# Performance work log

Measured on AMD Instinct MI355X. Metric: run time of the kernel, lower is better.

## Reference

```python
import jax, jax.numpy as jnp
import numpy as np

EPS = 1e-5


def layer_norm(x, g, b):
    mu = jnp.mean(x, axis=-1, keepdims=True)
    var = jnp.mean((x - mu) ** 2, axis=-1, keepdims=True)
    return (x - mu) * jax.lax.rsqrt(var + EPS) * g + b


def rel_enc_shift(arr):
    # Transformer-XL shift trick: [b,n,l,m] -> shifted [b,n,l,m]
    b, n, l, m = arr.shape
    arr = jnp.concatenate([arr, jnp.zeros((b, n, l, 1), arr.dtype)], axis=-1)
    arr = arr.reshape(b, n, -1)
    arr = arr[:, :, l - 1:-1].reshape(b, n, l, m)
    return arr


def setup_inputs() -> dict:
    key = jax.random.key(0)
    B, S, M, D, H = 2, 1024, 1024, 1024, 16
    F = S + M
    ks = jax.random.split(key, 16)
    sc = 0.02
    inp = {
        "inputs": jax.random.normal(ks[0], (B, S, D), jnp.float32),
        "mem": jax.random.normal(ks[1], (B, M, D), jnp.float32),
        "rel_enc": jax.random.normal(ks[2], (F, D), jnp.float32),
        # causal mask with memory: query i may attend keys j <= i + M; 1 = masked
        "mask": (jnp.arange(F)[None, :] > (jnp.arange(S)[:, None] + M)).astype(jnp.float32)[None, None],
        "ln1_g": jnp.ones((D,), jnp.float32), "ln1_b": jnp.zeros((D,), jnp.float32),
        "wq": jax.random.normal(ks[3], (D, D), jnp.float32) * sc,
        "wke": jax.random.normal(ks[4], (D, D), jnp.float32) * sc,
        "wkr": jax.random.normal(ks[5], (D, D), jnp.float32) * sc,
        "wv": jax.random.normal(ks[6], (D, D), jnp.float32) * sc,
        "wf": jax.random.normal(ks[7], (D, D), jnp.float32) * sc,
        "u_param": jax.random.normal(ks[8], (1, 1, H, D // H), jnp.float32) * 0.05,
        "v_param": jax.random.normal(ks[9], (1, 1, H, D // H), jnp.float32) * 0.05,
        "ln2_g": jnp.ones((D,), jnp.float32), "ln2_b": jnp.zeros((D,), jnp.float32),
        "w1": jax.random.normal(ks[10], (D, D), jnp.float32) * sc,
        "b1": jnp.zeros((D,), jnp.float32),
        "w2": jax.random.normal(ks[11], (D, D), jnp.float32) * sc,
        "b2": jnp.zeros((D,), jnp.float32),
        "wg1": jax.random.normal(ks[12], (D, D), jnp.float32) * sc,
        "bg1": jnp.zeros((D,), jnp.float32),
        "wg2": jax.random.normal(ks[13], (D, D), jnp.float32) * sc,
        "bg2": jnp.zeros((D,), jnp.float32),
    }
    return inp


def _block(inputs, mem, mask, rel_enc, ln1_g, ln1_b, wq, wke, wkr, wv, wf,
           u_param, v_param, ln2_g, ln2_b, w1, b1, w2, b2, wg1, bg1, wg2, bg2):
    B, S, D = inputs.shape
    H = u_param.shape[2]
    dh = D // H
    x_tilde = jnp.concatenate([jax.lax.stop_gradient(mem), inputs], axis=1)
    F = x_tilde.shape[1]
    x_tilde = layer_norm(x_tilde, ln1_g, ln1_b)
    x = x_tilde[:, -S:, :]
    q = (x @ wq).reshape(B, S, H, dh)
    k = (x_tilde @ wke).reshape(B, F, H, dh)
    v = (x_tilde @ wv).reshape(B, F, H, dh)
    A_C = jnp.einsum('bsnd,bfnd->bnsf', q + u_param, k)
    Q = (rel_enc @ wkr).reshape(F, H, dh)
    B_D = rel_enc_shift(jnp.einsum('bsnd,fnd->bnsf', q + v_param, Q))
    score = (A_C + B_D) / jnp.sqrt(jnp.float32(D)) + mask * -1e10
    attn = jax.nn.softmax(score, axis=-1)
    attention_loss = jnp.mean(jnp.max(attn, axis=(-1, -2)))
    ao = jnp.einsum('bnsf,bfnd->bsnd', attn, v).reshape(B, S, D)
    rmha_out = jax.nn.gelu(ao @ wf, approximate=False)
    # gating 1 (output gating): x + sigmoid(Wx+b)*y
    g1 = inputs + jax.nn.sigmoid(inputs @ wg1 + bg1) * rmha_out
    h = layer_norm(g1, ln2_g, ln2_b)
    h = jax.nn.gelu(h @ w1 + b1, approximate=False)
    h = jax.nn.gelu(h @ w2 + b2, approximate=False)
    out = g1 + jax.nn.sigmoid(g1 @ wg2 + bg2) * h
    return out, attn, attention_loss


def reference(inputs, mem, mask, rel_enc, ln1_g, ln1_b, wq, wke, wkr, wv, wf,
              u_param, v_param, ln2_g, ln2_b, w1, b1, w2, b2, wg1, bg1, wg2, bg2):
    return _block(inputs, mem, mask, rel_enc, ln1_g, ln1_b, wq, wke, wkr, wv, wf,
                  u_param, v_param, ln2_g, ln2_b, w1, b1, w2, b2, wg1, bg1, wg2, bg2)
```

## Files before the change

kernel.cpp:

```cpp
#include <hip/hip_runtime.h>
#include <hip/hip_bf16.h>


typedef __attribute__((ext_vector_type(8))) short bf16x8;
typedef __attribute__((ext_vector_type(4))) float f32x4;

#define MFMA16(a, b, c) __builtin_amdgcn_mfma_f32_16x16x32_bf16((a), (b), (c), 0, 0, 0)

__device__ __forceinline__ unsigned short f2bf(float f) {
  union { __hip_bfloat16 h; unsigned short u; } cv;
  cv.h = __float2bfloat16(f);
  return cv.u;
}

__device__ __forceinline__ float gelu_f(float x) {
  return 0.5f * x * (1.f + erff(x * 0.70710678118654752f));
}

struct W9 { const float* p[9]; };

__global__ __launch_bounds__(256) void k_init(
    const float* __restrict__ inputs, const float* __restrict__ mem,
    const float* __restrict__ rel_enc, const float* __restrict__ g1n,
    const float* __restrict__ b1n, W9 wp,
    unsigned short* __restrict__ xt, unsigned short* __restrict__ inb,
    unsigned short* __restrict__ reb, unsigned short* __restrict__ wT,
    float* __restrict__ amax) {
  int bid = blockIdx.x, tid = threadIdx.x;
  if (bid == 0 && tid < 32) amax[tid] = 0.f;
  if (bid < 4096) {
    __shared__ float red[8];
    int b = bid >> 11, fi = bid & 2047;
    const float* src = (fi < 1024)
        ? (mem + ((size_t)(b * 1024 + fi)) * 1024)
        : (inputs + ((size_t)(b * 1024 + fi - 1024)) * 1024);
    float4 x = ((const float4*)src)[tid];
    float s = x.x + x.y + x.z + x.w;
    float ss = x.x * x.x + x.y * x.y + x.z * x.z + x.w * x.w;
#pragma unroll
    for (int m = 32; m > 0; m >>= 1) {
      s += __shfl_down(s, m, 64);
      ss += __shfl_down(ss, m, 64);
    }
    int w = tid >> 6;
    if ((tid & 63) == 0) { red[w] = s; red[4 + w] = ss; }
    __syncthreads();
    s = red[0] + red[1] + red[2] + red[3];
    ss = red[4] + red[5] + red[6] + red[7];
    float mu = s * (1.f / 1024.f);
    float inv = rsqrtf(ss * (1.f / 1024.f) - mu * mu + 1e-5f);
    float4 g = ((const float4*)g1n)[tid];
    float4 bb = ((const float4*)b1n)[tid];
    ushort4 o;
    o.x = f2bf((x.x - mu) * inv * g.x + bb.x);
    o.y = f2bf((x.y - mu) * inv * g.y + bb.y);
    o.z = f2bf((x.z - mu) * inv * g.z + bb.z);
    o.w = f2bf((x.w - mu) * inv * g.w + bb.w);
    ((ushort4*)(xt + (size_t)bid * 1024))[tid] = o;
    if (fi >= 1024) {
      ushort4 r4;
      r4.x = f2bf(x.x); r4.y = f2bf(x.y); r4.z = f2bf(x.z); r4.w = f2bf(x.w);
      ((ushort4*)(inb + ((size_t)(b * 1024 + fi - 1024)) * 1024))[tid] = r4;
    }
  } else if (bid < 6144) {
    int r = bid - 4096;
    float4 x = ((const float4*)(rel_enc + (size_t)r * 1024))[tid];
    ushort4 o;
    o.x = f2bf(x.x); o.y = f2bf(x.y); o.z = f2bf(x.z); o.w = f2bf(x.w);
    ((ushort4*)(reb + (size_t)r * 1024))[tid] = o;
  } else {
    __shared__ float tl[64][65];
    int idx = bid - 6144;
    int m = idx >> 8;
    int t = idx & 255;
    int k0 = (t >> 4) << 6, n0 = (t & 15) << 6;
    const float* srcw = wp.p[m];
    int kr = tid >> 4, nc = (tid & 15) << 2;
#pragma unroll
    for (int i = 0; i < 4; ++i) {
      int krow = i * 16 + kr;
      float4 v = *(const float4*)(srcw + (size_t)(k0 + krow) * 1024 + n0 + nc);
      tl[nc + 0][krow] = v.x;
      tl[nc + 1][krow] = v.y;
      tl[nc + 2][krow] = v.z;
      tl[nc + 3][krow] = v.w;
    }
    __syncthreads();
    int n = tid >> 2, kc0 = (tid & 3) << 4;
    unsigned short* dst = wT + ((size_t)m << 20) + (size_t)(n0 + n) * 1024 + k0 + kc0;
#pragma unroll
    for (int q = 0; q < 4; ++q) {
      ushort4 o;
      o.x = f2bf(tl[n][kc0 + q * 4 + 0]);
      o.y = f2bf(tl[n][kc0 + q * 4 + 1]);
      o.z = f2bf(tl[n][kc0 + q * 4 + 2]);
      o.w = f2bf(tl[n][kc0 + q * 4 + 3]);
      *(ushort4*)(dst + q * 4) = o;
    }
  }
}

__global__ __launch_bounds__(256) void k_ln(
    const float* __restrict__ xin, const float* __restrict__ g1n,
    const float* __restrict__ b1n, unsigned short* __restrict__ outb) {
  __shared__ float red[8];
  int bid = blockIdx.x, tid = threadIdx.x;
  const float* src = xin + (size_t)bid * 1024;
  float4 x = ((const float4*)src)[tid];
  float s = x.x + x.y + x.z + x.w;
  float ss = x.x * x.x + x.y * x.y + x.z * x.z + x.w * x.w;
#pragma unroll
  for (int m = 32; m > 0; m >>= 1) {
    s += __shfl_down(s, m, 64);
    ss += __shfl_down(ss, m, 64);
  }
  int w = tid >> 6;
  if ((tid & 63) == 0) { red[w] = s; red[4 + w] = ss; }
  __syncthreads();
  s = red[0] + red[1] + red[2] + red[3];
  ss = red[4] + red[5] + red[6] + red[7];
  float mu = s * (1.f / 1024.f);
  float inv = rsqrtf(ss * (1.f / 1024.f) - mu * mu + 1e-5f);
  float4 g = ((const float4*)g1n)[tid];
  float4 bb = ((const float4*)b1n)[tid];
  ushort4 o;
  o.x = f2bf((x.x - mu) * inv * g.x + bb.x);
  o.y = f2bf((x.y - mu) * inv * g.y + bb.y);
  o.z = f2bf((x.z - mu) * inv * g.z + bb.z);
  o.w = f2bf((x.w - mu) * inv * g.w + bb.w);
  ((ushort4*)(outb + (size_t)bid * 1024))[tid] = o;
}

__device__ __forceinline__ int lds_u128(int r, int g) {
  return g * 128 + (r & ~7) + ((r ^ g) & 7);
}
template <int TM>
__device__ __forceinline__ int lds_uT(int r, int g) {
  return g * TM + (r & ~7) + ((r ^ g) & 7);
}

enum { EP_KV = 0, EP_QUV, EP_BF16, EP_GELU_F32, EP_GATE1,
       EP_GELU_B_BF16, EP_GELU_B_F32, EP_GATE2 };

template <int EP, int TM>
__global__ __launch_bounds__(256, 2) void k_gemm(
    const unsigned short* __restrict__ A, const unsigned short* __restrict__ Bw,
    int arow_add, int arow_mul,
    const float* __restrict__ bias, const float* __restrict__ auxA,
    const float* __restrict__ auxB, void* __restrict__ out0,
    void* __restrict__ out1) {
  constexpr int MI = TM / 16;
  constexpr int AU = TM / 32;
  __shared__ __align__(16) unsigned short As[2][TM * 64];
  __shared__ __align__(16) unsigned short Bs[2][128 * 64];
  int tid = threadIdx.x;
  int lane = tid & 63, wave = tid >> 6;
  int quad = lane >> 4, col = lane & 15;
  int bm = blockIdx.y, bn = blockIdx.x;
  f32x4 acc[MI][2] = {};
  int str = tid >> 3, stg = tid & 7;
  const unsigned short* aptr[AU];
  int au[AU];
  const unsigned short* bptr[4];
  int bu[4];
#pragma unroll
  for (int i = 0; i < AU; ++i) {
    int r = str + 32 * i;
    int gr = bm * TM + r;
    int ar = gr + arow_add + (gr >> 10) * arow_mul;
    aptr[i] = A + (size_t)ar * 1024 + stg * 8;
    au[i] = lds_uT<TM>(r, stg);
  }
#pragma unroll
  for (int i = 0; i < 4; ++i) {
    int r = str + 32 * i;
    bptr[i] = Bw + (size_t)(bn * 128 + r) * 1024 + stg * 8;
    bu[i] = lds_u128(r, stg);
  }
  uint4 av[AU], bv[4];
#pragma unroll
  for (int i = 0; i < AU; ++i) av[i] = *(const uint4*)(aptr[i]);
#pragma unroll
  for (int i = 0; i < 4; ++i) bv[i] = *(const uint4*)(bptr[i]);
#pragma unroll
  for (int i = 0; i < AU; ++i) ((uint4*)As[0])[au[i]] = av[i];
#pragma unroll
  for (int i = 0; i < 4; ++i) ((uint4*)Bs[0])[bu[i]] = bv[i];
  for (int kt = 0; kt < 16; ++kt) {
    __syncthreads();
    if (kt < 15) {
      int k0 = (kt + 1) * 64;
#pragma unroll
      for (int i = 0; i < AU; ++i) av[i] = *(const uint4*)(aptr[i] + k0);
#pragma unroll
      for (int i = 0; i < 4; ++i) bv[i] = *(const uint4*)(bptr[i] + k0);
    }
    int cur = kt & 1;
#pragma unroll
    for (int ks = 0; ks < 2; ++ks) {
      bf16x8 af[MI], bfr[2];
#pragma unroll
      for (int mi = 0; mi < MI; ++mi)
        af[mi] = ((const bf16x8*)As[cur])[lds_uT<TM>(mi * 16 + col, ks * 4 + quad)];
#pragma unroll
      for (int ni = 0; ni < 2; ++ni)
        bfr[ni] = ((const bf16x8*)Bs[cur])[lds_u128(wave * 32 + ni * 16 + col, ks * 4 + quad)];
#pragma unroll
      for (int mi = 0; mi < MI; ++mi)
#pragma unroll
        for (int ni = 0; ni < 2; ++ni)
          acc[mi][ni] = MFMA16(af[mi], bfr[ni], acc[mi][ni]);
    }
    if (kt < 15) {
      int nxt = cur ^ 1;
#pragma unroll
      for (int i = 0; i < AU; ++i) ((uint4*)As[nxt])[au[i]] = av[i];
#pragma unroll
      for (int i = 0; i < 4; ++i) ((uint4*)Bs[nxt])[bu[i]] = bv[i];
    }
  }
#pragma unroll
  for (int mi = 0; mi < MI; ++mi)
#pragma unroll
    for (int ni = 0; ni < 2; ++ni)
#pragma unroll
      for (int r = 0; r < 4; ++r) {
        int grow = bm * TM + mi * 16 + quad * 4 + r;
        int gcol = bn * 128 + wave * 32 + ni * 16 + col;
        float v = acc[mi][ni][r];
        size_t idx = (size_t)grow * 1024 + gcol;
        if constexpr (EP == EP_KV) {
          if (gcol < 1024) {
            ((unsigned short*)out0)[(size_t)grow * 1024 + gcol] = f2bf(v);
          } else {
            ((unsigned short*)out1)[(size_t)grow * 1024 + gcol - 1024] = f2bf(v);
          }
        } else if constexpr (EP == EP_QUV) {
          ((unsigned short*)out0)[idx] = f2bf(v + auxA[gcol]);
          ((unsigned short*)out1)[idx] = f2bf(v + auxB[gcol]);
        } else if constexpr (EP == EP_BF16) {
          ((unsigned short*)out0)[idx] = f2bf(v);
        } else if constexpr (EP == EP_GELU_F32) {
          ((float*)out0)[idx] = gelu_f(v);
        } else if constexpr (EP == EP_GATE1) {
          float a = v + bias[gcol];
          float sg = 1.f / (1.f + __expf(-a));
          float g1 = auxA[idx] + sg * auxB[idx];
          ((float*)out0)[idx] = g1;
          ((unsigned short*)out1)[idx] = f2bf(g1);
        } else if constexpr (EP == EP_GELU_B_BF16) {
          ((unsigned short*)out0)[idx] = f2bf(gelu_f(v + bias[gcol]));
        } else if constexpr (EP == EP_GELU_B_F32) {
          ((float*)out0)[idx] = gelu_f(v + bias[gcol]);
        } else {
          float a = v + bias[gcol];
          float sg = 1.f / (1.f + __expf(-a));
          ((float*)out0)[idx] = auxA[idx] + sg * auxB[idx];
        }
      }
}

__global__ __launch_bounds__(256) void k_tr(
    const unsigned short* __restrict__ v, unsigned short* __restrict__ vT) {
  __shared__ unsigned short tl[64][72];
  int bh = blockIdx.x, ft = blockIdx.y;
  int b = bh >> 4, h = bh & 15;
  int f0 = ft * 64;
  int tid = threadIdx.x;
  int fr = tid >> 2, c0 = (tid & 3) * 16;
  *(uint4*)&tl[fr][c0] =
      *(const uint4*)(v + ((size_t)(b * 2048 + f0 + fr)) * 1024 + h * 64 + c0);
  __syncthreads();
  int dr = tid >> 2, fc = (tid & 3) * 16;
  unsigned short* dst =
      vT + (((size_t)(b * 16 + h) * 64 + dr)) * 2048 + f0 + fc;
#pragma unroll
  for (int q = 0; q < 4; ++q) {
    ushort4 o;
    o.x = tl[fc + q * 4 + 0][dr];
    o.y = tl[fc + q * 4 + 1][dr];
    o.z = tl[fc + q * 4 + 2][dr];
    o.w = tl[fc + q * 4 + 3][dr];
    *(ushort4*)(dst + q * 4) = o;
  }
}

__global__ __launch_bounds__(256) void k_att(
    const unsigned short* __restrict__ qu, const unsigned short* __restrict__ qv,
    const unsigned short* __restrict__ kk, const unsigned short* __restrict__ vT,
    const unsigned short* __restrict__ Qr,
    float* __restrict__ attn, unsigned short* __restrict__ ao,
    float* __restrict__ rinvb, float* __restrict__ amax) {
  __shared__ __align__(16) unsigned short Pl[4][512];
  __shared__ __align__(16) float Ol[2][1024];
  __shared__ float Sl[4][16];
  __shared__ float Rinv[16];
  int tid = threadIdx.x, lane = tid & 63, wave = tid >> 6;
  int quad = lane >> 4, col = lane & 15;
  int bh = blockIdx.x, rt = blockIdx.y;
  int b = bh >> 4, h = bh & 15;
  int ri = rt * 16;

  bf16x8 quf[2], qvf[2];
  {
    const unsigned short* p0 = qu + ((size_t)(b * 1024 + ri + col)) * 1024 + h * 64 + quad * 8;
    quf[0] = *(const bf16x8*)p0;
    quf[1] = *(const bf16x8*)(p0 + 32);
    const unsigned short* p1 = qv + ((size_t)(b * 1024 + ri + col)) * 1024 + h * 64 + quad * 8;
    qvf[0] = *(const bf16x8*)p1;
    qvf[1] = *(const bf16x8*)(p1 + 32);
  }

  const unsigned short* qrbase = Qr + h * 64 + quad * 8;
  auto r_load = [&](int cbase, bf16x8& b0, bf16x8& b1) {
    int cr = cbase + col;
    cr = cr < 0 ? 0 : (cr > 2047 ? 2047 : cr);
    const unsigned short* p = qrbase + (size_t)cr * 1024;
    b0 = *(const bf16x8*)p;
    b1 = *(const bf16x8*)(p + 32);
  };
  auto r_mm = [&](bf16x8 b0, bf16x8 b1) -> f32x4 {
    f32x4 z = {0.f, 0.f, 0.f, 0.f};
    z = MFMA16(qvf[0], b0, z);
    z = MFMA16(qvf[1], b1, z);
    return z;
  };

  const unsigned short* kbase = kk + ((size_t)(b * 2048)) * 1024 + h * 64 + quad * 8;
  const unsigned short* vbase = vT + ((size_t)((b * 16 + h) * 64)) * 2048;
  float* arow0 = attn + ((size_t)bh * 1024 + ri + quad * 4) * 2048 + col;

  f32x4 o4[4] = {};
  f32x4 srow = {0.f, 0.f, 0.f, 0.f};
  f32x4 pm = {0.f, 0.f, 0.f, 0.f};
  int jmax = ri + 15 + 1024;
  int jlo = wave * 512;

  if (jlo <= jmax) {
    int hi = jmax < jlo + 511 ? jmax : jlo + 511;
    int nch = ((hi - jlo) >> 5) + 1;
    int cw = 1008 - ri + jlo;
    f32x4 Rcur;
    {
      bf16x8 rb0, rb1;
      r_load(cw, rb0, rb1);
      Rcur = r_mm(rb0, rb1);
    }
    for (int ch = 0; ch < nch; ++ch) {
      int j0 = jlo + ch * 32;
      bf16x8 ra0, ra1, rc0, rc1;
      r_load(cw + 16, ra0, ra1);
      r_load(cw + 32, rc0, rc1);
      const unsigned short* kp0 = kbase + (size_t)(j0 + col) * 1024;
      const unsigned short* kp1 = kbase + (size_t)(j0 + 16 + col) * 1024;
      bf16x8 k00 = *(const bf16x8*)kp0;
      bf16x8 k01 = *(const bf16x8*)(kp0 + 32);
      bf16x8 k10 = *(const bf16x8*)kp1;
      bf16x8 k11 = *(const bf16x8*)(kp1 + 32);
      int fb = j0 + quad * 8;
      bf16x8 vf[4];
#pragma unroll
      for (int ni = 0; ni < 4; ++ni)
        vf[ni] = *(const bf16x8*)(vbase + (size_t)(ni * 16 + col) * 2048 + fb);
      f32x4 Rn1 = r_mm(ra0, ra1);
      f32x4 Rn2 = r_mm(rc0, rc1);
      f32x4 ac0 = {0.f, 0.f, 0.f, 0.f};
      ac0 = MFMA16(quf[0], k00, ac0);
      ac0 = MFMA16(quf[1], k01, ac0);
      f32x4 ac1 = {0.f, 0.f, 0.f, 0.f};
      ac1 = MFMA16(quf[0], k10, ac1);
      ac1 = MFMA16(quf[1], k11, ac1);
#pragma unroll
      for (int r = 0; r < 4; ++r) {
        int w = 15 + col - quad * 4 - r;
        int src = quad * 16 + (w & 15);
        float bd0 = __shfl(Rcur[r], src, 64);
        float bd1 = __shfl(Rn1[r], src, 64);
        float bd = (w < 16) ? bd0 : bd1;
        float sc = (ac0[r] + bd) * 0.03125f;
        int masked = (j0 + col) > (ri + quad * 4 + r + 1024);
        float p = masked ? 0.f : __expf(sc);
        srow[r] += p;
        pm[r] = fmaxf(pm[r], p);
        arow0[(size_t)r * 2048 + j0] = p;
        Pl[wave][(quad * 4 + r) * 32 + col] = f2bf(p);
      }
#pragma unroll
      for (int r = 0; r < 4; ++r) {
        int w = 15 + col - quad * 4 - r;
        int src = quad * 16 + (w & 15);
        float bd0 = __shfl(Rn1[r], src, 64);
        float bd1 = __shfl(Rn2[r], src, 64);
        float bd = (w < 16) ? bd0 : bd1;
        float sc = (ac1[r] + bd) * 0.03125f;
        int masked = (j0 + 16 + col) > (ri + quad * 4 + r + 1024);
        float p = masked ? 0.f : __expf(sc);
        srow[r] += p;
        pm[r] = fmaxf(pm[r], p);
        arow0[(size_t)r * 2048 + j0 + 16] = p;
        Pl[wave][(quad * 4 + r) * 32 + 16 + col] = f2bf(p);
      }
      asm volatile("s_waitcnt lgkmcnt(0)" ::: "memory");
      bf16x8 pf = *(const bf16x8*)&Pl[wave][col * 32 + quad * 8];
#pragma unroll
      for (int ni = 0; ni < 4; ++ni) o4[ni] = MFMA16(pf, vf[ni], o4[ni]);
      Rcur = Rn2;
      cw += 32;
    }
  }
#pragma unroll
  for (int r = 0; r < 4; ++r) {
    float v = srow[r], m = pm[r];
    v += __shfl_xor(v, 1, 64);  m = fmaxf(m, __shfl_xor(m, 1, 64));
    v += __shfl_xor(v, 2, 64);  m = fmaxf(m, __shfl_xor(m, 2, 64));
    v += __shfl_xor(v, 4, 64);  m = fmaxf(m, __shfl_xor(m, 4, 64));
    v += __shfl_xor(v, 8, 64);  m = fmaxf(m, __shfl_xor(m, 8, 64));
    srow[r] = v; pm[r] = m;
  }
  if (col == 0) {
#pragma unroll
    for (int r = 0; r < 4; ++r) Sl[wave][quad * 4 + r] = srow[r];
  }
  if (wave >= 2) {
#pragma unroll
    for (int ni = 0; ni < 4; ++ni)
#pragma unroll
      for (int r = 0; r < 4; ++r)
        Ol[wave - 2][(quad * 4 + r) * 64 + ni * 16 + col] = o4[ni][r];
  }
  __syncthreads();
  if (tid < 16) {
    float rv = 1.f / (Sl[0][tid] + Sl[1][tid] + Sl[2][tid] + Sl[3][tid]);
    Rinv[tid] = rv;
    rinvb[(size_t)bh * 1024 + ri + tid] = rv;
  }
  if (wave < 2) {
#pragma unroll
    for (int ni = 0; ni < 4; ++ni)
#pragma unroll
      for (int r = 0; r < 4; ++r) {
        int ix = (quad * 4 + r) * 64 + ni * 16 + col;
        o4[ni][r] += Ol[wave][ix];
        if (wave == 1) Ol[1][ix] = o4[ni][r];
      }
  }
  __syncthreads();
  if (wave == 0) {
#pragma unroll
    for (int ni = 0; ni < 4; ++ni)
#pragma unroll
      for (int r = 0; r < 4; ++r) {
        int ix = (quad * 4 + r) * 64 + ni * 16 + col;
        o4[ni][r] += Ol[1][ix];
        Ol[0][ix] = o4[ni][r];
      }
  }
  __syncthreads();
  {
    int row = tid >> 4, d0 = (tid & 15) << 2;
    float4 ov = *(const float4*)&Ol[0][row * 64 + d0];
    float rv = Rinv[row];
    ushort4 o;
    o.x = f2bf(ov.x * rv); o.y = f2bf(ov.y * rv);
    o.z = f2bf(ov.z * rv); o.w = f2bf(ov.w * rv);
    *(ushort4*)(ao + ((size_t)(b * 1024 + ri + row)) * 1024 + h * 64 + d0) = o;
  }
  float pmax = 0.f;
#pragma unroll
  for (int r = 0; r < 4; ++r) pmax = fmaxf(pmax, pm[r] * Rinv[quad * 4 + r]);
  pmax = fmaxf(pmax, __shfl_xor(pmax, 16, 64));
  pmax = fmaxf(pmax, __shfl_xor(pmax, 32, 64));
  if (lane == 0) atomicMax((int*)(amax + bh), __float_as_int(pmax));
}

__global__ __launch_bounds__(256) void k_norm(
    float* __restrict__ attn, const float* __restrict__ rinvb) {
  int gr = blockIdx.x;
  int s = gr & 1023;
  float rv = rinvb[gr];
  int j0 = threadIdx.x * 8;
  int lim = s + 1024;
  float* row = attn + (size_t)gr * 2048 + j0;
  float4 a = {0.f, 0.f, 0.f, 0.f}, b4 = {0.f, 0.f, 0.f, 0.f};
  if (j0 <= lim) {
    a = ((const float4*)row)[0];
    b4 = ((const float4*)row)[1];
  }
  float4 oa, ob;
  oa.x = (j0 + 0 <= lim) ? a.x * rv : 0.f;
  oa.y = (j0 + 1 <= lim) ? a.y * rv : 0.f;
  oa.z = (j0 + 2 <= lim) ? a.z * rv : 0.f;
  oa.w = (j0 + 3 <= lim) ? a.w * rv : 0.f;
  ob.x = (j0 + 4 <= lim) ? b4.x * rv : 0.f;
  ob.y = (j0 + 5 <= lim) ? b4.y * rv : 0.f;
  ob.z = (j0 + 6 <= lim) ? b4.z * rv : 0.f;
  ob.w = (j0 + 7 <= lim) ? b4.w * rv : 0.f;
  ((float4*)row)[0] = oa;
  ((float4*)row)[1] = ob;
}

__global__ void k_loss(const float* __restrict__ amax, float* __restrict__ out) {
  int l = threadIdx.x;
  float v = (l < 32) ? amax[l] : 0.f;
  v += __shfl_xor(v, 1, 64);
  v += __shfl_xor(v, 2, 64);
  v += __shfl_xor(v, 4, 64);
  v += __shfl_xor(v, 8, 64);
  v += __shfl_xor(v, 16, 64);
  v += __shfl_xor(v, 32, 64);
  if (l == 0) out[0] = v * (1.f / 32.f);
}

extern "C" void kernel_launch(void* const* d_in, const int* in_sizes, int n_in,
                              void* d_out, int out_size, void* d_ws, size_t ws_size,
                              hipStream_t stream) {
  (void)in_sizes; (void)n_in; (void)out_size; (void)ws_size;
  const float* inputs = (const float*)d_in[0];
  const float* mem    = (const float*)d_in[1];
  const float* rel    = (const float*)d_in[2];
  const float* ln1g   = (const float*)d_in[4];
  const float* ln1b   = (const float*)d_in[5];
  const float* wq     = (const float*)d_in[6];
  const float* wke    = (const float*)d_in[7];
  const float* wkr    = (const float*)d_in[8];
  const float* wv     = (const float*)d_in[9];
  const float* wf     = (const float*)d_in[10];
  const float* up     = (const float*)d_in[11];
  const float* vp     = (const float*)d_in[12];
  const float* ln2g   = (const float*)d_in[13];
  const float* ln2b   = (const float*)d_in[14];
  const float* w1     = (const float*)d_in[15];
  const float* b1     = (const float*)d_in[16];
  const float* w2     = (const float*)d_in[17];
  const float* b2     = (const float*)d_in[18];
  const float* wg1    = (const float*)d_in[19];
  const float* bg1    = (const float*)d_in[20];
  const float* wg2    = (const float*)d_in[21];
  const float* bg2    = (const float*)d_in[22];

  char* ws = (char*)d_ws;
  unsigned short* wT  = (unsigned short*)(ws);
  unsigned short* xt  = (unsigned short*)(ws + 18874368);
  unsigned short* inb = (unsigned short*)(ws + 27262976);
  unsigned short* reb = (unsigned short*)(ws + 31457280);
  unsigned short* kb  = (unsigned short*)(ws + 35651584);
  unsigned short* vTb = (unsigned short*)(ws + 44040192);
  unsigned short* qub = (unsigned short*)(ws + 52428800);
  unsigned short* qvb = (unsigned short*)(ws + 56623104);
  unsigned short* Qrb = (unsigned short*)(ws + 60817408);
  float* amax         = (float*)(ws + 65011712);
  float* rinvb        = (float*)(ws + 65012736);
  unsigned short* vb = qub;
  float* rmha = (float*)xt;
  unsigned short* aob = reb;
  float* g1f = (float*)kb;
  float* h2f = (float*)vTb;
  unsigned short* g1b = qub;
  unsigned short* h0b = qvb;
  unsigned short* h1b = Qrb;

  float* outp  = (float*)d_out;
  float* attnp = outp + 2097152;
  float* lossp = outp + 69206016;

  W9 wp;
  wp.p[0] = wq;  wp.p[1] = wke; wp.p[2] = wv;  wp.p[3] = wkr; wp.p[4] = wf;
  wp.p[5] = w1;  wp.p[6] = w2;  wp.p[7] = wg1; wp.p[8] = wg2;

  k_init<<<8448, 256, 0, stream>>>(inputs, mem, rel, ln1g, ln1b, wp,
                                   xt, inb, reb, wT, amax);
  k_gemm<EP_KV, 64><<<dim3(16, 64), 256, 0, stream>>>(
      xt, wT + (1u << 20), 0, 0, nullptr, nullptr, nullptr, kb, vb);
  k_tr<<<dim3(32, 32), 256, 0, stream>>>(vb, vTb);
  k_gemm<EP_QUV, 32><<<dim3(8, 64), 256, 0, stream>>>(
      xt, wT, 1024, 1024, nullptr, up, vp, qub, qvb);
  k_gemm<EP_BF16, 32><<<dim3(8, 64), 256, 0, stream>>>(
      reb, wT + 3u * (1u << 20), 0, 0, nullptr, nullptr, nullptr, Qrb, nullptr);
  k_att<<<dim3(32, 64), 256, 0, stream>>>(qub, qvb, kb, vTb, Qrb,
                                          attnp, aob, rinvb, amax);
  k_norm<<<32768, 256, 0, stream>>>(attnp, rinvb);
  k_gemm<EP_GELU_F32, 32><<<dim3(8, 64), 256, 0, stream>>>(
      aob, wT + 4u * (1u << 20), 0, 0, nullptr, nullptr, nullptr, rmha, nullptr);
  k_gemm<EP_GATE1, 32><<<dim3(8, 64), 256, 0, stream>>>(
      inb, wT + 7u * (1u << 20), 0, 0, bg1, inputs, rmha, g1f, g1b);
  k_ln<<<2048, 256, 0, stream>>>(g1f, ln2g, ln2b, h0b);
  k_gemm<EP_GELU_B_BF16, 32><<<dim3(8, 64), 256, 0, stream>>>(
      h0b, wT + 5u * (1u << 20), 0, 0, b1, nullptr, nullptr, h1b, nullptr);
  k_gemm<EP_GELU_B_F32, 32><<<dim3(8, 64), 256, 0, stream>>>(
      h1b, wT + 6u * (1u << 20), 0, 0, b2, nullptr, nullptr, h2f, nullptr);
  k_gemm<EP_GATE2, 32><<<dim3(8, 64), 256, 0, stream>>>(
      g1b, wT + 8u * (1u << 20), 0, 0, bg2, g1f, h2f, outp, nullptr);
  k_loss<<<1, 64, 0, stream>>>(amax, lossp);
}
```

Before: 784.8 us.

## Fuse softmax normalization into attention kernel via LDS-resident probability rows

The attention kernel now keeps the full 16x2048 tile of unnormalized probabilities in shared memory as bf16. After the row sums are known, it writes the normalized, masked attention matrix to global memory in a single pass. This removes the separate normalization kernel, the unnormalized fp32 store and its later read and rewrite of the large attention output. The trade-offs are that the returned attention weights are now rounded through bf16, and the roughly 66KB LDS buffer limits how many blocks can run per CU.

```diff
diff --git a/kernel.cpp b/kernel.cpp
--- a/kernel.cpp
+++ b/kernel.cpp
@@ -11,6 +11,10 @@
   union { __hip_bfloat16 h; unsigned short u; } cv;
   cv.h = __float2bfloat16(f);
   return cv.u;
+}
+
+__device__ __forceinline__ float bf2f(unsigned short u) {
+  return __uint_as_float((unsigned)u << 16);
 }
 
 __device__ __forceinline__ float gelu_f(float x) {
@@ -290,8 +294,8 @@
     const unsigned short* __restrict__ kk, const unsigned short* __restrict__ vT,
     const unsigned short* __restrict__ Qr,
     float* __restrict__ attn, unsigned short* __restrict__ ao,
-    float* __restrict__ rinvb, float* __restrict__ amax) {
-  __shared__ __align__(16) unsigned short Pl[4][512];
+    float* __restrict__ amax) {
+  __shared__ __align__(16) unsigned short Pb[16][2056];
   __shared__ __align__(16) float Ol[2][1024];
   __shared__ float Sl[4][16];
   __shared__ float Rinv[16];
@@ -328,7 +332,6 @@
 
   const unsigned short* kbase = kk + ((size_t)(b * 2048)) * 1024 + h * 64 + quad * 8;
   const unsigned short* vbase = vT + ((size_t)((b * 16 + h) * 64)) * 2048;
-  float* arow0 = attn + ((size_t)bh * 1024 + ri + quad * 4) * 2048 + col;
 
   f32x4 o4[4] = {};
   f32x4 srow = {0.f, 0.f, 0.f, 0.f};
@@ -382,8 +385,7 @@
         float p = masked ? 0.f : __expf(sc);
         srow[r] += p;
         pm[r] = fmaxf(pm[r], p);
-        arow0[(size_t)r * 2048 + j0] = p;
-        Pl[wave][(quad * 4 + r) * 32 + col] = f2bf(p);
+        Pb[quad * 4 + r][j0 + col] = f2bf(p);
       }
 #pragma unroll
       for (int r = 0; r < 4; ++r) {
@@ -397,11 +399,10 @@
         float p = masked ? 0.f : __expf(sc);
         srow[r] += p;
         pm[r] = fmaxf(pm[r], p);
-        arow0[(size_t)r * 2048 + j0 + 16] = p;
-        Pl[wave][(quad * 4 + r) * 32 + 16 + col] = f2bf(p);
+        Pb[quad * 4 + r][j0 + 16 + col] = f2bf(p);
       }
       asm volatile("s_waitcnt lgkmcnt(0)" ::: "memory");
-      bf16x8 pf = *(const bf16x8*)&Pl[wave][col * 32 + quad * 8];
+      bf16x8 pf = *(const bf16x8*)&Pb[col][j0 + quad * 8];
 #pragma unroll
       for (int ni = 0; ni < 4; ++ni) o4[ni] = MFMA16(pf, vf[ni], o4[ni]);
       Rcur = Rn2;
@@ -432,7 +433,6 @@
   if (tid < 16) {
     float rv = 1.f / (Sl[0][tid] + Sl[1][tid] + Sl[2][tid] + Sl[3][tid]);
     Rinv[tid] = rv;
-    rinvb[(size_t)bh * 1024 + ri + tid] = rv;
   }
   if (wave < 2) {
 #pragma unroll
@@ -471,32 +471,25 @@
   pmax = fmaxf(pmax, __shfl_xor(pmax, 16, 64));
   pmax = fmaxf(pmax, __shfl_xor(pmax, 32, 64));
   if (lane == 0) atomicMax((int*)(amax + bh), __float_as_int(pmax));
-}
-
-__global__ __launch_bounds__(256) void k_norm(
-    float* __restrict__ attn, const float* __restrict__ rinvb) {
-  int gr = blockIdx.x;
-  int s = gr & 1023;
-  float rv = rinvb[gr];
-  int j0 = threadIdx.x * 8;
-  int lim = s + 1024;
-  float* row = attn + (size_t)gr * 2048 + j0;
-  float4 a = {0.f, 0.f, 0.f, 0.f}, b4 = {0.f, 0.f, 0.f, 0.f};
-  if (j0 <= lim) {
-    a = ((const float4*)row)[0];
-    b4 = ((const float4*)row)[1];
-  }
-  float4 oa, ob;
-  oa.x = (j0 + 0 <= lim) ? a.x * rv : 0.f;
-  oa.y = (j0 + 1 <= lim) ? a.y * rv : 0.f;
-  oa.z = (j0 + 2 <= lim) ? a.z * rv : 0.f;
-  oa.w = (j0 + 3 <= lim) ? a.w * rv : 0.f;
-  ob.x = (j0 + 4 <= lim) ? b4.x * rv : 0.f;
-  ob.y = (j0 + 5 <= lim) ? b4.y * rv : 0.f;
-  ob.z = (j0 + 6 <= lim) ? b4.z * rv : 0.f;
-  ob.w = (j0 + 7 <= lim) ? b4.w * rv : 0.f;
-  ((float4*)row)[0] = oa;
-  ((float4*)row)[1] = ob;
+
+  {
+    float* abase = attn + ((size_t)bh * 1024 + ri) * 2048;
+#pragma unroll 4
+    for (int it = 0; it < 32; ++it) {
+      int idx = it * 256 + tid;
+      int row = idx >> 9;
+      int j = (idx & 511) << 2;
+      float rv = Rinv[row];
+      int lim = ri + row + 1024;
+      ushort4 p4 = *(const ushort4*)&Pb[row][j];
+      float4 o;
+      o.x = (j + 0 <= lim) ? bf2f(p4.x) * rv : 0.f;
+      o.y = (j + 1 <= lim) ? bf2f(p4.y) * rv : 0.f;
+      o.z = (j + 2 <= lim) ? bf2f(p4.z) * rv : 0.f;
+      o.w = (j + 3 <= lim) ? bf2f(p4.w) * rv : 0.f;
+      *(float4*)(abase + (size_t)row * 2048 + j) = o;
+    }
+  }
 }
 
 __global__ void k_loss(const float* __restrict__ amax, float* __restrict__ out) {
@@ -549,7 +542,6 @@
   unsigned short* qvb = (unsigned short*)(ws + 56623104);
   unsigned short* Qrb = (unsigned short*)(ws + 60817408);
   float* amax         = (float*)(ws + 65011712);
-  float* rinvb        = (float*)(ws + 65012736);
   unsigned short* vb = qub;
   float* rmha = (float*)xt;
   unsigned short* aob = reb;
@@ -577,8 +569,7 @@
   k_gemm<EP_BF16, 32><<<dim3(8, 64), 256, 0, stream>>>(
       reb, wT + 3u * (1u << 20), 0, 0, nullptr, nullptr, nullptr, Qrb, nullptr);
   k_att<<<dim3(32, 64), 256, 0, stream>>>(qub, qvb, kb, vTb, Qrb,
-                                          attnp, aob, rinvb, amax);
-  k_norm<<<32768, 256, 0, stream>>>(attnp, rinvb);
+                                          attnp, aob, amax);
   k_gemm<EP_GELU_F32, 32><<<dim3(8, 64), 256, 0, stream>>>(
       aob, wT + 4u * (1u << 20), 0, 0, nullptr, nullptr, nullptr, rmha, nullptr);
   k_gemm<EP_GATE1, 32><<<dim3(8, 64), 256, 0, stream>>>(
```

After: 715.4 us. -8.8%, faster.
